# Kernel optimization log

Measured on AMD Instinct MI355X. Metric: run time of the kernel, lower is better.

The kernel has to match this reference:

```python
import jax, jax.numpy as jnp
import numpy as np

N, E, B = 50000, 800000, 2000
EMB, FEAT, L, NTASK = 300, 512, 5, 1
EPS = 1e-5


def setup_inputs() -> dict:
    key = jax.random.key(0)
    ks = jax.random.split(key, 40)
    s = 0.05
    d = {
        'x': jax.random.randint(ks[0], (N, 42), 0, 3),
        'edge_index': jax.random.randint(ks[1], (2, E), 0, N),
        'edge_attr': jax.random.randint(ks[2], (E, 10), 0, 3),
        'batch': jnp.sort(jax.random.randint(ks[3], (N,), 0, B)),
        'x_add': jax.random.normal(ks[4], (B, 200), jnp.float32),
        # atom embeddings
        'atom_e1': jax.random.normal(ks[5], (120, EMB), jnp.float32) * s,
        'atom_e2': jax.random.normal(ks[6], (3, EMB), jnp.float32) * s,
        'atom_w3': jax.random.normal(ks[7], (40, EMB), jnp.float32) * s,
        'atom_b3': jnp.zeros((EMB,), jnp.float32),
        # per-layer GINEConv params (stacked over L layers)
        'edge_e1': jax.random.normal(ks[8], (L, 6, EMB), jnp.float32) * s,
        'edge_e2': jax.random.normal(ks[9], (L, 4, EMB), jnp.float32) * s,
        'edge_w3': jax.random.normal(ks[10], (L, 8, EMB), jnp.float32) * s,
        'edge_b3': jnp.zeros((L, EMB), jnp.float32),
        'mlp_w1': jax.random.normal(ks[11], (L, EMB, 2 * EMB), jnp.float32) * s,
        'mlp_b1': jnp.zeros((L, 2 * EMB), jnp.float32),
        'mlp_w2': jax.random.normal(ks[12], (L, 2 * EMB, EMB), jnp.float32) * s,
        'mlp_b2': jnp.zeros((L, EMB), jnp.float32),
        'bn_g': jnp.ones((L, EMB), jnp.float32),
        'bn_b': jnp.zeros((L, EMB), jnp.float32),
        # feat_lin: emb_dim + 200 -> feat_dim
        'feat_w': jax.random.normal(ks[13], (EMB + 200, FEAT), jnp.float32) * s,
        'feat_b': jnp.zeros((FEAT,), jnp.float32),
        # pred head: 512->256 softplus, 256->256 softplus, 256->1
        'pw1': jax.random.normal(ks[14], (FEAT, FEAT // 2), jnp.float32) * s,
        'pb1': jnp.zeros((FEAT // 2,), jnp.float32),
        'pw2': jax.random.normal(ks[15], (FEAT // 2, FEAT // 2), jnp.float32) * s,
        'pb2': jnp.zeros((FEAT // 2,), jnp.float32),
        'pw3': jax.random.normal(ks[16], (FEAT // 2, NTASK), jnp.float32) * s,
        'pb3': jnp.zeros((NTASK,), jnp.float32),
    }
    return d


def reference(x, edge_index, edge_attr, batch, x_add,
              atom_e1, atom_e2, atom_w3, atom_b3,
              edge_e1, edge_e2, edge_w3, edge_b3,
              mlp_w1, mlp_b1, mlp_w2, mlp_b2, bn_g, bn_b,
              feat_w, feat_b, pw1, pb1, pw2, pb2, pw3, pb3):
    n = x.shape[0]
    nb = x_add.shape[0]

    # node embedding: emb(atom_type) + emb(chirality) + Linear(40 float feats)
    h = (atom_e1[x[:, 0]] + atom_e2[x[:, 1]]
         + x[:, 2:].astype(jnp.float32) @ atom_w3 + atom_b3)

    # add self loops once (same for every layer); self-loop attr: col0=4, rest 0
    loop = jnp.arange(n, dtype=edge_index.dtype)
    src = jnp.concatenate([edge_index[0], loop])
    dst = jnp.concatenate([edge_index[1], loop])
    ea0 = jnp.concatenate([edge_attr[:, 0], jnp.full((n,), 4, edge_attr.dtype)])
    ea1 = jnp.concatenate([edge_attr[:, 1], jnp.zeros((n,), edge_attr.dtype)])
    eaf = jnp.concatenate([edge_attr[:, 2:].astype(jnp.float32),
                           jnp.zeros((n, 8), jnp.float32)], axis=0)

    for l in range(L):
        e_emb = edge_e1[l][ea0] + edge_e2[l][ea1] + eaf @ edge_w3[l] + edge_b3[l]
        msg = h[src] + e_emb                              # [E+N, EMB] gather
        agg = jax.ops.segment_sum(msg, dst, num_segments=n)  # scatter-add
        h = jnp.maximum(agg @ mlp_w1[l] + mlp_b1[l], 0.0) @ mlp_w2[l] + mlp_b2[l]
        # BatchNorm1d (training-mode batch stats, biased var)
        mu = jnp.mean(h, axis=0)
        var = jnp.mean((h - mu) ** 2, axis=0)
        h = (h - mu) * jax.lax.rsqrt(var + EPS) * bn_g[l] + bn_b[l]
        if l != L - 1:
            h = jnp.maximum(h, 0.0)
    h_node = h

    # global mean pool per graph
    sums = jax.ops.segment_sum(h_node, batch, num_segments=nb)
    cnt = jax.ops.segment_sum(jnp.ones((n, 1), h_node.dtype), batch, num_segments=nb)
    pooled = sums / jnp.maximum(cnt, 1.0)

    g = jnp.concatenate([pooled, x_add], axis=1) @ feat_w + feat_b
    g = jax.nn.softplus(g @ pw1 + pb1)
    g = jax.nn.softplus(g @ pw2 + pb2)
    pred = g @ pw3 + pb3
    return h_node, pred
```

## Files before the change

### kernel.cpp

```cpp
#include <hip/hip_runtime.h>
#include <stdint.h>

#define NN 50000
#define EE 800000
#define BG 2000
#define EMB 300
#define HP 320
#define YP 640
#define MPAD 50048
#define MHEAD 2048
#define NLAYER 5

typedef __attribute__((ext_vector_type(8))) _Float16 f16x8;
typedef __attribute__((ext_vector_type(4))) float f32x4;

__device__ __forceinline__ _Float16 f2h(float f) { return (_Float16)f; }

__global__ void k_tconv_all(const float* __restrict__ mw1, const float* __restrict__ mw2,
        const float* __restrict__ fw, const float* __restrict__ pw1, const float* __restrict__ pw2,
        _Float16* __restrict__ w1t, _Float16* __restrict__ w2t, _Float16* __restrict__ fwt,
        _Float16* __restrict__ p1t, _Float16* __restrict__ p2t) {
    int job = blockIdx.x;
    const float* src; _Float16* dst; int K, Ns, Kp, Np;
    if (job < 5)       { src = mw1 + (size_t)job * EMB * 2 * EMB; dst = w1t + (size_t)job * YP * HP; K = EMB; Ns = 2 * EMB; Kp = HP; Np = YP; }
    else if (job < 10) { int l = job - 5; src = mw2 + (size_t)l * 2 * EMB * EMB; dst = w2t + (size_t)l * HP * YP; K = 2 * EMB; Ns = EMB; Kp = YP; Np = HP; }
    else if (job == 10){ src = fw;  dst = fwt; K = 500; Ns = 512; Kp = 512; Np = 512; }
    else if (job == 11){ src = pw1; dst = p1t; K = 512; Ns = 256; Kp = 512; Np = 256; }
    else               { src = pw2; dst = p2t; K = 256; Ns = 256; Kp = 256; Np = 256; }
    int total = Kp * Np;
    for (int idx = blockIdx.y * 256 + threadIdx.x; idx < total; idx += gridDim.y * 256) {
        int n = idx / Kp, k = idx - n * Kp;
        float v = (n < Ns && k < K) ? src[(size_t)k * Ns + n] : 0.f;
        dst[idx] = f2h(v);
    }
}

__global__ void k_padbias_all(const float* __restrict__ mb1, const float* __restrict__ mb2,
                              float* __restrict__ b1p, float* __restrict__ b2p) {
    int idx = blockIdx.x * 256 + threadIdx.x;
    if (idx < NLAYER * YP) {
        int l = idx / YP, c = idx - l * YP;
        b1p[idx] = (c < 2 * EMB) ? mb1[(size_t)l * 2 * EMB + c] : 0.f;
    } else if (idx < NLAYER * YP + NLAYER * HP) {
        int j = idx - NLAYER * YP; int l = j / HP, c = j - l * HP;
        b2p[j] = (c < EMB) ? mb2[(size_t)l * EMB + c] : 0.f;
    }
}

__global__ void k_prep(int* __restrict__ deg, int* __restrict__ cursor,
                       float* __restrict__ psum, float* __restrict__ psq) {
    int i = blockIdx.x * blockDim.x + threadIdx.x;
    if (i < NN) { deg[i] = 0; cursor[i] = 0; }
    if (i < NLAYER * HP) { psum[i] = 0.f; psq[i] = 0.f; }
}

__global__ __launch_bounds__(256) void k_embed(const int* __restrict__ x,
        const float* __restrict__ ae1, const float* __restrict__ ae2,
        const float* __restrict__ aw3, const float* __restrict__ ab3,
        _Float16* __restrict__ h2) {
    int node = blockIdx.x * 4 + (threadIdx.x >> 6);
    int lane = threadIdx.x & 63;
    if (node >= MPAD) return;
    _Float16* outr = h2 + (size_t)node * HP;
    if (node >= NN) {
        #pragma unroll
        for (int j = 0; j < 5; j++) outr[lane + 64 * j] = (_Float16)0.f;
        return;
    }
    const int* xr = x + (size_t)node * 42;
    int x0 = xr[0], x1 = xr[1];
    float acc[5];
    #pragma unroll
    for (int j = 0; j < 5; j++) {
        int c = lane + 64 * j;
        acc[j] = (j < 4 || c < EMB)
               ? (ab3[c] + ae1[(size_t)x0 * EMB + c] + ae2[(size_t)x1 * EMB + c]) : 0.f;
    }
    for (int k = 0; k < 40; k++) {
        float xv = (float)xr[2 + k];
        #pragma unroll
        for (int j = 0; j < 5; j++) {
            int c = lane + 64 * j;
            if (j < 4 || c < EMB) acc[j] = fmaf(xv, aw3[(size_t)k * EMB + c], acc[j]);
        }
    }
    #pragma unroll
    for (int j = 0; j < 5; j++) {
        int c = lane + 64 * j;
        outr[c] = (j < 4 || c < EMB) ? f2h(acc[j]) : (_Float16)0.f;
    }
}

__global__ void k_deg(const int* __restrict__ ei, int* __restrict__ deg) {
    int e = blockIdx.x * blockDim.x + threadIdx.x;
    if (e < EE) atomicAdd(&deg[ei[EE + e]], 1);
}

__global__ __launch_bounds__(1024) void k_scan(const int* __restrict__ deg,
                                               int* __restrict__ rowptr) {
    __shared__ int part[1024];
    int t = threadIdx.x;
    const int chunk = (NN + 1023) / 1024;
    int i0 = t * chunk;
    int i1 = min(i0 + chunk, NN);
    int s = 0;
    for (int i = i0; i < i1; i++) s += deg[i];
    part[t] = s;
    __syncthreads();
    for (int off = 1; off < 1024; off <<= 1) {
        int v = part[t];
        int u = (t >= off) ? part[t - off] : 0;
        __syncthreads();
        part[t] = v + u;
        __syncthreads();
    }
    int run = (t > 0) ? part[t - 1] : 0;
    for (int i = i0; i < i1; i++) { rowptr[i] = run; run += deg[i]; }
    if (t == 1023) rowptr[NN] = part[1023];
}

__global__ void k_fill(const int* __restrict__ ei, const int* __restrict__ ea,
                       const int* __restrict__ rowptr, int* __restrict__ cursor,
                       int* __restrict__ col, unsigned int* __restrict__ eattr) {
    int e = blockIdx.x * blockDim.x + threadIdx.x;
    if (e < EE) {
        int d = ei[EE + e];
        int pos = rowptr[d] + atomicAdd(&cursor[d], 1);
        col[pos] = ei[e];
        unsigned int p = (unsigned int)ea[e * 10 + 0] | ((unsigned int)ea[e * 10 + 1] << 2);
        #pragma unroll
        for (int j = 0; j < 8; j++) p |= (unsigned int)ea[e * 10 + 2 + j] << (4 + 2 * j);
        eattr[pos] = p;
    }
}

__global__ __launch_bounds__(256) void k_sortrows(const int* __restrict__ rowptr,
                                                  int* __restrict__ col) {
    int node = blockIdx.x * 4 + (threadIdx.x >> 6);
    int lane = threadIdx.x & 63;
    if (node >= NN) return;
    int beg = rowptr[node], end = rowptr[node + 1];
    int deg = end - beg;
    if (deg <= 1 || deg > 64) return;
    int v = (lane < deg) ? col[beg + lane] : 0x7fffffff;
    #pragma unroll
    for (int k = 2; k <= 64; k <<= 1) {
        #pragma unroll
        for (int j = k >> 1; j > 0; j >>= 1) {
            int v2 = __shfl_xor(v, j);
            bool keepMin = (((lane & j) == 0) == ((lane & k) == 0));
            v = keepMin ? min(v, v2) : max(v, v2);
        }
    }
    if (lane < deg) col[beg + lane] = v;
}

__global__ __launch_bounds__(256) void k_stats(const int* __restrict__ rowptr,
        const unsigned int* __restrict__ eattr, int* __restrict__ stat) {
    int node = blockIdx.x * 4 + (threadIdx.x >> 6);
    int lane = threadIdx.x & 63;
    if (node >= NN) return;
    int beg = rowptr[node], end = rowptr[node + 1];
    int c0 = 0, c1 = 0, c2 = 0, d1 = 0, d2 = 0;
    int s[8] = {0, 0, 0, 0, 0, 0, 0, 0};
    for (int e = beg + lane; e < end; e += 64) {
        unsigned int p = eattr[e];
        unsigned int a0 = p & 3u, a1 = (p >> 2) & 3u;
        c0 += (a0 == 0); c1 += (a0 == 1); c2 += (a0 == 2);
        d1 += (a1 == 1); d2 += (a1 == 2);
        #pragma unroll
        for (int j = 0; j < 8; j++) s[j] += (int)((p >> (4 + 2 * j)) & 3u);
    }
    #pragma unroll
    for (int off = 32; off; off >>= 1) {
        c0 += __shfl_down(c0, off); c1 += __shfl_down(c1, off); c2 += __shfl_down(c2, off);
        d1 += __shfl_down(d1, off); d2 += __shfl_down(d2, off);
        #pragma unroll
        for (int j = 0; j < 8; j++) s[j] += __shfl_down(s[j], off);
    }
    if (lane == 0) {
        int dg = end - beg;
        int* st = stat + (size_t)node * 20;
        st[0] = c0; st[1] = c1; st[2] = c2; st[3] = 0; st[4] = 1; st[5] = 0;
        st[6] = dg - d1 - d2 + 1; st[7] = d1; st[8] = d2; st[9] = 0;
        #pragma unroll
        for (int j = 0; j < 8; j++) st[10 + j] = s[j];
        st[18] = dg + 1; st[19] = 0;
    }
}

#define AGG_CHUNK 160
template<int RELU>
__global__ __launch_bounds__(320) void k_agg(const _Float16* __restrict__ h2,
        const float* __restrict__ psum, const float* __restrict__ psq,
        const float* __restrict__ bng, const float* __restrict__ bnb,
        const int* __restrict__ stat, const int* __restrict__ rowptr,
        const int* __restrict__ col,
        const float* __restrict__ ee1, const float* __restrict__ ee2,
        const float* __restrict__ ew3, const float* __restrict__ eb3,
        _Float16* __restrict__ agg, int layer) {
    int i = blockIdx.x;
    int tid = threadIdx.x;
    if (i >= NN) { agg[(size_t)i * HP + tid] = (_Float16)0.f; return; }
    __shared__ int ss[20];
    __shared__ int sc[AGG_CHUNK];
    if (tid < 20) ss[tid] = stat[(size_t)i * 20 + tid];
    int c = tid;
    bool ch = c < EMB;
    float scl = 0.f, sft = 0.f;
    if (ch) {
        if (RELU) {
            float mu = psum[(size_t)(layer - 1) * HP + c] * (1.f / NN);
            float var = psq[(size_t)(layer - 1) * HP + c] * (1.f / NN) - mu * mu;
            float g = bng[(size_t)(layer - 1) * EMB + c] * rsqrtf(var + 1e-5f);
            scl = g; sft = bnb[(size_t)(layer - 1) * EMB + c] - mu * g;
        } else { scl = 1.f; sft = 0.f; }
    }
    __syncthreads();
    float acc = 0.f;
    if (ch) {
        const float* e1 = ee1 + (size_t)layer * 6 * EMB;
        const float* e2 = ee2 + (size_t)layer * 4 * EMB;
        const float* w3 = ew3 + (size_t)layer * 8 * EMB;
        float v = eb3[(size_t)layer * EMB + c] * (float)ss[18] + e1[4 * EMB + c];
        v = fmaf((float)ss[0], e1[c], v);
        v = fmaf((float)ss[1], e1[EMB + c], v);
        v = fmaf((float)ss[2], e1[2 * EMB + c], v);
        v = fmaf((float)ss[6], e2[c], v);
        v = fmaf((float)ss[7], e2[EMB + c], v);
        v = fmaf((float)ss[8], e2[2 * EMB + c], v);
        #pragma unroll
        for (int k = 0; k < 8; k++) v = fmaf((float)ss[10 + k], w3[k * EMB + c], v);
        float t = fmaf((float)h2[(size_t)i * HP + c], scl, sft);
        if (RELU) t = fmaxf(t, 0.f);
        acc = v + t;
    }
    int beg = rowptr[i], end = rowptr[i + 1];
    for (int e0 = beg; e0 < end; e0 += AGG_CHUNK) {
        int m = min(AGG_CHUNK, end - e0);
        __syncthreads();
        if (tid < m) sc[tid] = col[e0 + tid];
        __syncthreads();
        if (ch) {
            #pragma unroll 4
            for (int e = 0; e < m; e++) {
                float t = fmaf((float)h2[(size_t)sc[e] * HP + c], scl, sft);
                if (RELU) t = fmaxf(t, 0.f);
                acc += t;
            }
        }
    }
    agg[(size_t)i * HP + tid] = ch ? f2h(acc) : (_Float16)0.f;
}

__global__ __launch_bounds__(256) void k_gemm(const _Float16* __restrict__ A, int lda,
        const _Float16* __restrict__ Wt, int ldw, const float* __restrict__ bias,
        _Float16* __restrict__ C, int ldc, int K, int act, int gridY,
        float* __restrict__ psum, float* __restrict__ psq) {
    __shared__ _Float16 As[2][128 * 32];
    __shared__ _Float16 Bs[2][64 * 32];
    int nwg = gridDim.x;
    int q = nwg >> 3, r = nwg & 7;
    int xcd = blockIdx.x & 7, idx = blockIdx.x >> 3;
    int wg = ((xcd < r) ? xcd * (q + 1) : r * (q + 1) + (xcd - r) * q) + idx;
    int bx = wg / gridY, by = wg - bx * gridY;
    size_t rowBase = (size_t)bx * 128;
    int colBase = by * 64;

    int tid = threadIdx.x, lane = tid & 63, wid = tid >> 6;
    int wr = wid >> 1, wc = wid & 1;
    int srow = tid >> 2, schunk = tid & 3;
    int gchunk = schunk ^ ((srow >> 1) & 3);
    const _Float16* Ab  = A + (rowBase + srow) * (size_t)lda + (gchunk << 3);
    const _Float16* Ab2 = Ab + (size_t)64 * lda;
    const _Float16* Bb  = Wt + ((size_t)colBase + srow) * ldw + (gchunk << 3);
    int ldsbase = wid << 9;

    int lr = lane & 15, lg = lane >> 4;
    int lswz = (lr >> 1) & 3;
    int aoff[4], boff[2];
    #pragma unroll
    for (int m = 0; m < 4; m++) { int rr = wr * 64 + m * 16 + lr; aoff[m] = rr * 32 + ((lg ^ lswz) << 3); }
    #pragma unroll
    for (int n = 0; n < 2; n++) { int rr = wc * 32 + n * 16 + lr; boff[n] = rr * 32 + ((lg ^ lswz) << 3); }

    f32x4 acc[4][2];
    #pragma unroll
    for (int m = 0; m < 4; m++)
        #pragma unroll
        for (int n = 0; n < 2; n++) acc[m][n] = (f32x4){0.f, 0.f, 0.f, 0.f};

    auto stage = [&](int buf, int kt) {
        int o = kt << 5;
        __builtin_amdgcn_global_load_lds(
            (const __attribute__((address_space(1))) void*)(Ab + o),
            (__attribute__((address_space(3))) void*)&As[buf][ldsbase], 16, 0, 0);
        __builtin_amdgcn_global_load_lds(
            (const __attribute__((address_space(1))) void*)(Ab2 + o),
            (__attribute__((address_space(3))) void*)&As[buf][64 * 32 + ldsbase], 16, 0, 0);
        __builtin_amdgcn_global_load_lds(
            (const __attribute__((address_space(1))) void*)(Bb + o),
            (__attribute__((address_space(3))) void*)&Bs[buf][ldsbase], 16, 0, 0);
    };

    int nk = K >> 5;
    stage(0, 0);
    __syncthreads();
    int cur = 0;
    for (int kt = 0; kt < nk; ++kt) {
        if (kt + 1 < nk) stage(cur ^ 1, kt + 1);
        f16x8 af[4], bfr[2];
        #pragma unroll
        for (int m = 0; m < 4; m++) af[m] = *(const f16x8*)&As[cur][aoff[m]];
        #pragma unroll
        for (int n = 0; n < 2; n++) bfr[n] = *(const f16x8*)&Bs[cur][boff[n]];
        #pragma unroll
        for (int m = 0; m < 4; m++)
            #pragma unroll
            for (int n = 0; n < 2; n++)
                acc[m][n] = __builtin_amdgcn_mfma_f32_16x16x32_f16(af[m], bfr[n], acc[m][n], 0, 0, 0);
        __syncthreads();
        cur ^= 1;
    }

    bool dostats = (psum != nullptr);
    float sstat[2] = {0.f, 0.f}, qstat[2] = {0.f, 0.f};
    #pragma unroll
    for (int m = 0; m < 4; m++) {
        #pragma unroll
        for (int n = 0; n < 2; n++) {
            int colg = colBase + wc * 32 + n * 16 + lr;
            float bv = bias[colg];
            #pragma unroll
            for (int rj = 0; rj < 4; rj++) {
                size_t rowg = rowBase + wr * 64 + m * 16 + lg * 4 + rj;
                float v = acc[m][n][rj] + bv;
                if (act == 1) v = fmaxf(v, 0.f);
                else if (act == 2) v = (v > 0.f) ? v + log1pf(expf(-v)) : log1pf(expf(v));
                C[rowg * ldc + colg] = f2h(v);
                if (dostats && rowg < NN) { sstat[n] += v; qstat[n] += v * v; }
            }
        }
    }
    if (dostats) {
        #pragma unroll
        for (int n = 0; n < 2; n++) {
            float s_ = sstat[n], q_ = qstat[n];
            s_ += __shfl_xor(s_, 16); q_ += __shfl_xor(q_, 16);
            s_ += __shfl_xor(s_, 32); q_ += __shfl_xor(q_, 32);
            if (lane < 16) {
                int colg = colBase + wc * 32 + n * 16 + lr;
                atomicAdd(&psum[colg], s_);
                atomicAdd(&psq[colg], q_);
            }
        }
    }
}

__global__ __launch_bounds__(256) void k_bn_apply(const _Float16* __restrict__ h2,
        const float* __restrict__ psum, const float* __restrict__ psq,
        const float* __restrict__ bng, const float* __restrict__ bnb,
        float* __restrict__ out) {
    int node = blockIdx.x * 4 + (threadIdx.x >> 6);
    int lane = threadIdx.x & 63;
    if (node >= NN) return;
    const float* ps = psum + (size_t)(NLAYER - 1) * HP;
    const float* pq = psq  + (size_t)(NLAYER - 1) * HP;
    const float* g_ = bng + (size_t)(NLAYER - 1) * EMB;
    const float* b_ = bnb + (size_t)(NLAYER - 1) * EMB;
    #pragma unroll
    for (int j = 0; j < 5; j++) {
        int c = lane + 64 * j;
        if (j < 4 || c < EMB) {
            float mu = ps[c] * (1.f / NN);
            float var = pq[c] * (1.f / NN) - mu * mu;
            float g = g_[c] * rsqrtf(var + 1e-5f);
            out[(size_t)node * EMB + c] =
                fmaf((float)h2[(size_t)node * HP + c], g, b_[c] - mu * g);
        }
    }
}

__global__ __launch_bounds__(512) void k_pool(const float* __restrict__ hn,
        const int* __restrict__ batch, const float* __restrict__ x_add,
        _Float16* __restrict__ hin) {
    int b = blockIdx.x, c = threadIdx.x;
    if (b >= BG) { hin[(size_t)b * 512 + c] = (_Float16)0.f; return; }
    __shared__ int sb[2];
    if (c < 2) {
        int target = b + c;
        int lo = 0, hi = NN;
        while (lo < hi) { int mid = (lo + hi) >> 1; if (batch[mid] < target) lo = mid + 1; else hi = mid; }
        sb[c] = lo;
    }
    __syncthreads();
    float v = 0.f;
    if (c < EMB) {
        int s = sb[0], e = sb[1];
        float a = 0.f;
        for (int i = s; i < e; i++) a += hn[(size_t)i * EMB + c];
        v = a / (float)max(e - s, 1);
    } else if (c < EMB + 200) {
        v = x_add[(size_t)b * 200 + (c - EMB)];
    }
    hin[(size_t)b * 512 + c] = f2h(v);
}

__global__ __launch_bounds__(64) void k_pred(const _Float16* __restrict__ g3,
        const float* __restrict__ pw3, const float* __restrict__ pb3, float* __restrict__ out) {
    int row = blockIdx.x;
    int lane = threadIdx.x;
    float s = 0.f;
    #pragma unroll
    for (int t = 0; t < 4; t++) {
        int k = lane * 4 + t;
        s += (float)g3[(size_t)row * 256 + k] * pw3[k];
    }
    #pragma unroll
    for (int off = 32; off; off >>= 1) s += __shfl_down(s, off);
    if (lane == 0) out[row] = s + pb3[0];
}

extern "C" void kernel_launch(void* const* d_in, const int* in_sizes, int n_in,
                              void* d_out, int out_size, void* d_ws, size_t ws_size,
                              hipStream_t stream) {
    const int*   x     = (const int*)d_in[0];
    const int*   ei    = (const int*)d_in[1];
    const int*   ea    = (const int*)d_in[2];
    const int*   batch = (const int*)d_in[3];
    const float* x_add = (const float*)d_in[4];
    const float* ae1   = (const float*)d_in[5];
    const float* ae2   = (const float*)d_in[6];
    const float* aw3   = (const float*)d_in[7];
    const float* ab3   = (const float*)d_in[8];
    const float* ee1   = (const float*)d_in[9];
    const float* ee2   = (const float*)d_in[10];
    const float* ew3   = (const float*)d_in[11];
    const float* eb3   = (const float*)d_in[12];
    const float* mw1   = (const float*)d_in[13];
    const float* mb1   = (const float*)d_in[14];
    const float* mw2   = (const float*)d_in[15];
    const float* mb2   = (const float*)d_in[16];
    const float* bng   = (const float*)d_in[17];
    const float* bnb   = (const float*)d_in[18];
    const float* fw    = (const float*)d_in[19];
    const float* fb    = (const float*)d_in[20];
    const float* pw1   = (const float*)d_in[21];
    const float* pb1   = (const float*)d_in[22];
    const float* pw2   = (const float*)d_in[23];
    const float* pb2   = (const float*)d_in[24];
    const float* pw3   = (const float*)d_in[25];
    const float* pb3   = (const float*)d_in[26];
    (void)in_sizes; (void)n_in; (void)out_size; (void)ws_size;
    float* out = (float*)d_out;

    char* p = (char*)d_ws;
    auto take = [&](size_t bytes) -> char* {
        char* r = p; p += (bytes + 255) & ~(size_t)255; return r;
    };
    _Float16*  h2   = (_Float16*)take((size_t)MPAD * HP * 2);
    _Float16*  agg  = (_Float16*)take((size_t)MPAD * HP * 2);
    _Float16*  y1   = (_Float16*)take((size_t)MPAD * YP * 2);
    _Float16*  w1t  = (_Float16*)take((size_t)NLAYER * YP * HP * 2);
    _Float16*  w2t  = (_Float16*)take((size_t)NLAYER * HP * YP * 2);
    _Float16*  fwt  = (_Float16*)take((size_t)512 * 512 * 2);
    _Float16*  p1t  = (_Float16*)take((size_t)256 * 512 * 2);
    _Float16*  p2t  = (_Float16*)take((size_t)256 * 256 * 2);
    float* b1p    = (float*)take((size_t)NLAYER * YP * 4);
    float* b2p    = (float*)take((size_t)NLAYER * HP * 4);
    int* deg      = (int*)take((size_t)NN * 4);
    int* cursor   = (int*)take((size_t)NN * 4);
    int* rowptr   = (int*)take((size_t)(NN + 1) * 4);
    int* col      = (int*)take((size_t)EE * 4);
    unsigned int* eattr = (unsigned int*)take((size_t)EE * 4);
    int* stat     = (int*)take((size_t)NN * 20 * 4);
    float* psum   = (float*)take((size_t)NLAYER * HP * 4);
    float* psq    = (float*)take((size_t)NLAYER * HP * 4);
    char* hb = (char*)y1;
    _Float16* hin = (_Float16*)hb;  hb += (size_t)MHEAD * 512 * 2;
    _Float16* g1  = (_Float16*)hb;  hb += (size_t)MHEAD * 512 * 2;
    _Float16* g2  = (_Float16*)hb;  hb += (size_t)MHEAD * 256 * 2;
    _Float16* g3  = (_Float16*)hb;

    k_prep<<<(NN + 255) / 256, 256, 0, stream>>>(deg, cursor, psum, psq);
    k_tconv_all<<<dim3(13, 1024), 256, 0, stream>>>(mw1, mw2, fw, pw1, pw2, w1t, w2t, fwt, p1t, p2t);
    k_padbias_all<<<19, 256, 0, stream>>>(mb1, mb2, b1p, b2p);
    k_embed<<<(MPAD + 3) / 4, 256, 0, stream>>>(x, ae1, ae2, aw3, ab3, h2);
    k_deg<<<(EE + 255) / 256, 256, 0, stream>>>(ei, deg);
    k_scan<<<1, 1024, 0, stream>>>(deg, rowptr);
    k_fill<<<(EE + 255) / 256, 256, 0, stream>>>(ei, ea, rowptr, cursor, col, eattr);
    k_sortrows<<<(NN + 3) / 4, 256, 0, stream>>>(rowptr, col);
    k_stats<<<(NN + 3) / 4, 256, 0, stream>>>(rowptr, eattr, stat);

    const int MT = MPAD / 128;
    for (int l = 0; l < NLAYER; l++) {
        if (l == 0)
            k_agg<0><<<MPAD, 320, 0, stream>>>(h2, psum, psq, bng, bnb,
                stat, rowptr, col, ee1, ee2, ew3, eb3, agg, l);
        else
            k_agg<1><<<MPAD, 320, 0, stream>>>(h2, psum, psq, bng, bnb,
                stat, rowptr, col, ee1, ee2, ew3, eb3, agg, l);
        k_gemm<<<MT * (YP / 64), 256, 0, stream>>>(
            agg, HP, w1t + (size_t)l * YP * HP, HP, b1p + (size_t)l * YP,
            y1, YP, HP, 1, YP / 64, nullptr, nullptr);
        k_gemm<<<MT * (HP / 64), 256, 0, stream>>>(
            y1, YP, w2t + (size_t)l * HP * YP, YP, b2p + (size_t)l * HP,
            h2, HP, YP, 0, HP / 64, psum + (size_t)l * HP, psq + (size_t)l * HP);
    }
    k_bn_apply<<<(NN + 3) / 4, 256, 0, stream>>>(h2, psum, psq, bng, bnb, out);

    k_pool<<<MHEAD, 512, 0, stream>>>(out, batch, x_add, hin);
    k_gemm<<<(MHEAD / 128) * (512 / 64), 256, 0, stream>>>(hin, 512, fwt, 512, fb, g1, 512, 512, 0, 512 / 64, nullptr, nullptr);
    k_gemm<<<(MHEAD / 128) * (256 / 64), 256, 0, stream>>>(g1, 512, p1t, 512, pb1, g2, 256, 512, 2, 256 / 64, nullptr, nullptr);
    k_gemm<<<(MHEAD / 128) * (256 / 64), 256, 0, stream>>>(g2, 256, p2t, 256, pb2, g3, 256, 256, 2, 256 / 64, nullptr, nullptr);
    k_pred<<<BG, 64, 0, stream>>>(g3, pw3, pb3, out + (size_t)NN * EMB);
}
```

Before: 1.815 ms.

## Widen GEMM tiles to 128x128, unroll aggregation gathers, drop row sorting

The GEMM tile grows from 128x64 to 128x128, so each wave holds a 4x4 grid of MFMA accumulators. The padded N dimension is masked with an Nvalid bound, and the W2 transpose is padded to 384 rows so it covers three 128-wide column tiles. The aggregation kernel now loads neighbour indices straight from global memory and issues eight gathers at a time instead of staging them through shared memory with barriers. The per-row column sort kernel is removed. This changes the summation order, and dropping the sort may hurt gather locality, while the larger tiles raise register pressure and give the second GEMM fewer blocks.

```diff
diff --git a/kernel.cpp b/kernel.cpp
--- a/kernel.cpp
+++ b/kernel.cpp
@@ -7,6 +7,7 @@
 #define EMB 300
 #define HP 320
 #define YP 640
+#define W2ROWS 384
 #define MPAD 50048
 #define MHEAD 2048
 #define NLAYER 5
@@ -23,7 +24,7 @@
     int job = blockIdx.x;
     const float* src; _Float16* dst; int K, Ns, Kp, Np;
     if (job < 5)       { src = mw1 + (size_t)job * EMB * 2 * EMB; dst = w1t + (size_t)job * YP * HP; K = EMB; Ns = 2 * EMB; Kp = HP; Np = YP; }
-    else if (job < 10) { int l = job - 5; src = mw2 + (size_t)l * 2 * EMB * EMB; dst = w2t + (size_t)l * HP * YP; K = 2 * EMB; Ns = EMB; Kp = YP; Np = HP; }
+    else if (job < 10) { int l = job - 5; src = mw2 + (size_t)l * 2 * EMB * EMB; dst = w2t + (size_t)l * W2ROWS * YP; K = 2 * EMB; Ns = EMB; Kp = YP; Np = W2ROWS; }
     else if (job == 10){ src = fw;  dst = fwt; K = 500; Ns = 512; Kp = 512; Np = 512; }
     else if (job == 11){ src = pw1; dst = p1t; K = 512; Ns = 256; Kp = 512; Np = 256; }
     else               { src = pw2; dst = p2t; K = 256; Ns = 256; Kp = 256; Np = 256; }
@@ -134,27 +135,6 @@
     }
 }
 
-__global__ __launch_bounds__(256) void k_sortrows(const int* __restrict__ rowptr,
-                                                  int* __restrict__ col) {
-    int node = blockIdx.x * 4 + (threadIdx.x >> 6);
-    int lane = threadIdx.x & 63;
-    if (node >= NN) return;
-    int beg = rowptr[node], end = rowptr[node + 1];
-    int deg = end - beg;
-    if (deg <= 1 || deg > 64) return;
-    int v = (lane < deg) ? col[beg + lane] : 0x7fffffff;
-    #pragma unroll
-    for (int k = 2; k <= 64; k <<= 1) {
-        #pragma unroll
-        for (int j = k >> 1; j > 0; j >>= 1) {
-            int v2 = __shfl_xor(v, j);
-            bool keepMin = (((lane & j) == 0) == ((lane & k) == 0));
-            v = keepMin ? min(v, v2) : max(v, v2);
-        }
-    }
-    if (lane < deg) col[beg + lane] = v;
-}
-
 __global__ __launch_bounds__(256) void k_stats(const int* __restrict__ rowptr,
         const unsigned int* __restrict__ eattr, int* __restrict__ stat) {
     int node = blockIdx.x * 4 + (threadIdx.x >> 6);
@@ -189,7 +169,6 @@
     }
 }
 
-#define AGG_CHUNK 160
 template<int RELU>
 __global__ __launch_bounds__(320) void k_agg(const _Float16* __restrict__ h2,
         const float* __restrict__ psum, const float* __restrict__ psq,
@@ -203,7 +182,6 @@
     int tid = threadIdx.x;
     if (i >= NN) { agg[(size_t)i * HP + tid] = (_Float16)0.f; return; }
     __shared__ int ss[20];
-    __shared__ int sc[AGG_CHUNK];
     if (tid < 20) ss[tid] = stat[(size_t)i * 20 + tid];
     int c = tid;
     bool ch = c < EMB;
@@ -231,41 +209,52 @@
         v = fmaf((float)ss[8], e2[2 * EMB + c], v);
         #pragma unroll
         for (int k = 0; k < 8; k++) v = fmaf((float)ss[10 + k], w3[k * EMB + c], v);
+        acc = v;
+    }
+    {
         float t = fmaf((float)h2[(size_t)i * HP + c], scl, sft);
         if (RELU) t = fmaxf(t, 0.f);
-        acc = v + t;
+        acc += t;
     }
     int beg = rowptr[i], end = rowptr[i + 1];
-    for (int e0 = beg; e0 < end; e0 += AGG_CHUNK) {
-        int m = min(AGG_CHUNK, end - e0);
-        __syncthreads();
-        if (tid < m) sc[tid] = col[e0 + tid];
-        __syncthreads();
-        if (ch) {
-            #pragma unroll 4
-            for (int e = 0; e < m; e++) {
-                float t = fmaf((float)h2[(size_t)sc[e] * HP + c], scl, sft);
-                if (RELU) t = fmaxf(t, 0.f);
-                acc += t;
-            }
+    int e = beg;
+    for (; e + 8 <= end; e += 8) {
+        int cb[8];
+        #pragma unroll
+        for (int t = 0; t < 8; t++) cb[t] = col[e + t];
+        float vb[8];
+        #pragma unroll
+        for (int t = 0; t < 8; t++) vb[t] = (float)h2[(size_t)cb[t] * HP + c];
+        float tb[8];
+        #pragma unroll
+        for (int t = 0; t < 8; t++) {
+            float tt = fmaf(vb[t], scl, sft);
+            if (RELU) tt = fmaxf(tt, 0.f);
+            tb[t] = tt;
         }
-    }
-    agg[(size_t)i * HP + tid] = ch ? f2h(acc) : (_Float16)0.f;
+        acc += ((tb[0] + tb[1]) + (tb[2] + tb[3])) + ((tb[4] + tb[5]) + (tb[6] + tb[7]));
+    }
+    for (; e < end; ++e) {
+        float tt = fmaf((float)h2[(size_t)col[e] * HP + c], scl, sft);
+        if (RELU) tt = fmaxf(tt, 0.f);
+        acc += tt;
+    }
+    agg[(size_t)i * HP + tid] = f2h(acc);
 }
 
 __global__ __launch_bounds__(256) void k_gemm(const _Float16* __restrict__ A, int lda,
         const _Float16* __restrict__ Wt, int ldw, const float* __restrict__ bias,
-        _Float16* __restrict__ C, int ldc, int K, int act, int gridY,
+        _Float16* __restrict__ C, int ldc, int Nvalid, int K, int act, int gridY,
         float* __restrict__ psum, float* __restrict__ psq) {
     __shared__ _Float16 As[2][128 * 32];
-    __shared__ _Float16 Bs[2][64 * 32];
+    __shared__ _Float16 Bs[2][128 * 32];
     int nwg = gridDim.x;
     int q = nwg >> 3, r = nwg & 7;
     int xcd = blockIdx.x & 7, idx = blockIdx.x >> 3;
     int wg = ((xcd < r) ? xcd * (q + 1) : r * (q + 1) + (xcd - r) * q) + idx;
     int bx = wg / gridY, by = wg - bx * gridY;
     size_t rowBase = (size_t)bx * 128;
-    int colBase = by * 64;
+    int colBase = by * 128;
 
     int tid = threadIdx.x, lane = tid & 63, wid = tid >> 6;
     int wr = wid >> 1, wc = wid & 1;
@@ -274,21 +263,22 @@
     const _Float16* Ab  = A + (rowBase + srow) * (size_t)lda + (gchunk << 3);
     const _Float16* Ab2 = Ab + (size_t)64 * lda;
     const _Float16* Bb  = Wt + ((size_t)colBase + srow) * ldw + (gchunk << 3);
+    const _Float16* Bb2 = Bb + (size_t)64 * ldw;
     int ldsbase = wid << 9;
 
     int lr = lane & 15, lg = lane >> 4;
     int lswz = (lr >> 1) & 3;
-    int aoff[4], boff[2];
+    int aoff[4], boff[4];
     #pragma unroll
     for (int m = 0; m < 4; m++) { int rr = wr * 64 + m * 16 + lr; aoff[m] = rr * 32 + ((lg ^ lswz) << 3); }
     #pragma unroll
-    for (int n = 0; n < 2; n++) { int rr = wc * 32 + n * 16 + lr; boff[n] = rr * 32 + ((lg ^ lswz) << 3); }
-
-    f32x4 acc[4][2];
+    for (int n = 0; n < 4; n++) { int rr = wc * 64 + n * 16 + lr; boff[n] = rr * 32 + ((lg ^ lswz) << 3); }
+
+    f32x4 acc[4][4];
     #pragma unroll
     for (int m = 0; m < 4; m++)
         #pragma unroll
-        for (int n = 0; n < 2; n++) acc[m][n] = (f32x4){0.f, 0.f, 0.f, 0.f};
+        for (int n = 0; n < 4; n++) acc[m][n] = (f32x4){0.f, 0.f, 0.f, 0.f};
 
     auto stage = [&](int buf, int kt) {
         int o = kt << 5;
@@ -301,6 +291,9 @@
         __builtin_amdgcn_global_load_lds(
             (const __attribute__((address_space(1))) void*)(Bb + o),
             (__attribute__((address_space(3))) void*)&Bs[buf][ldsbase], 16, 0, 0);
+        __builtin_amdgcn_global_load_lds(
+            (const __attribute__((address_space(1))) void*)(Bb2 + o),
+            (__attribute__((address_space(3))) void*)&Bs[buf][64 * 32 + ldsbase], 16, 0, 0);
     };
 
     int nk = K >> 5;
@@ -309,49 +302,45 @@
     int cur = 0;
     for (int kt = 0; kt < nk; ++kt) {
         if (kt + 1 < nk) stage(cur ^ 1, kt + 1);
-        f16x8 af[4], bfr[2];
+        f16x8 af[4], bf[4];
         #pragma unroll
         for (int m = 0; m < 4; m++) af[m] = *(const f16x8*)&As[cur][aoff[m]];
         #pragma unroll
-        for (int n = 0; n < 2; n++) bfr[n] = *(const f16x8*)&Bs[cur][boff[n]];
+        for (int n = 0; n < 4; n++) bf[n] = *(const f16x8*)&Bs[cur][boff[n]];
         #pragma unroll
         for (int m = 0; m < 4; m++)
             #pragma unroll
-            for (int n = 0; n < 2; n++)
-                acc[m][n] = __builtin_amdgcn_mfma_f32_16x16x32_f16(af[m], bfr[n], acc[m][n], 0, 0, 0);
+            for (int n = 0; n < 4; n++)
+                acc[m][n] = __builtin_amdgcn_mfma_f32_16x16x32_f16(af[m], bf[n], acc[m][n], 0, 0, 0);
         __syncthreads();
         cur ^= 1;
     }
 
     bool dostats = (psum != nullptr);
-    float sstat[2] = {0.f, 0.f}, qstat[2] = {0.f, 0.f};
-    #pragma unroll
-    for (int m = 0; m < 4; m++) {
-        #pragma unroll
-        for (int n = 0; n < 2; n++) {
-            int colg = colBase + wc * 32 + n * 16 + lr;
-            float bv = bias[colg];
+    #pragma unroll
+    for (int n = 0; n < 4; n++) {
+        int colg = colBase + wc * 64 + n * 16 + lr;
+        bool cok = colg < Nvalid;
+        float bv = cok ? bias[colg] : 0.f;
+        float sstat = 0.f, qstat = 0.f;
+        #pragma unroll
+        for (int m = 0; m < 4; m++) {
             #pragma unroll
             for (int rj = 0; rj < 4; rj++) {
                 size_t rowg = rowBase + wr * 64 + m * 16 + lg * 4 + rj;
                 float v = acc[m][n][rj] + bv;
                 if (act == 1) v = fmaxf(v, 0.f);
                 else if (act == 2) v = (v > 0.f) ? v + log1pf(expf(-v)) : log1pf(expf(v));
-                C[rowg * ldc + colg] = f2h(v);
-                if (dostats && rowg < NN) { sstat[n] += v; qstat[n] += v * v; }
+                if (cok) C[rowg * ldc + colg] = f2h(v);
+                if (dostats && rowg < NN) { sstat += v; qstat += v * v; }
             }
         }
-    }
-    if (dostats) {
-        #pragma unroll
-        for (int n = 0; n < 2; n++) {
-            float s_ = sstat[n], q_ = qstat[n];
-            s_ += __shfl_xor(s_, 16); q_ += __shfl_xor(q_, 16);
-            s_ += __shfl_xor(s_, 32); q_ += __shfl_xor(q_, 32);
-            if (lane < 16) {
-                int colg = colBase + wc * 32 + n * 16 + lr;
-                atomicAdd(&psum[colg], s_);
-                atomicAdd(&psq[colg], q_);
+        if (dostats) {
+            sstat += __shfl_xor(sstat, 16); qstat += __shfl_xor(qstat, 16);
+            sstat += __shfl_xor(sstat, 32); qstat += __shfl_xor(qstat, 32);
+            if (lane < 16 && cok) {
+                atomicAdd(&psum[colg], sstat);
+                atomicAdd(&psq[colg], qstat);
             }
         }
     }
@@ -462,7 +451,7 @@
     _Float16*  agg  = (_Float16*)take((size_t)MPAD * HP * 2);
     _Float16*  y1   = (_Float16*)take((size_t)MPAD * YP * 2);
     _Float16*  w1t  = (_Float16*)take((size_t)NLAYER * YP * HP * 2);
-    _Float16*  w2t  = (_Float16*)take((size_t)NLAYER * HP * YP * 2);
+    _Float16*  w2t  = (_Float16*)take((size_t)NLAYER * W2ROWS * YP * 2);
     _Float16*  fwt  = (_Float16*)take((size_t)512 * 512 * 2);
     _Float16*  p1t  = (_Float16*)take((size_t)256 * 512 * 2);
     _Float16*  p2t  = (_Float16*)take((size_t)256 * 256 * 2);
@@ -489,7 +478,6 @@
     k_deg<<<(EE + 255) / 256, 256, 0, stream>>>(ei, deg);
     k_scan<<<1, 1024, 0, stream>>>(deg, rowptr);
     k_fill<<<(EE + 255) / 256, 256, 0, stream>>>(ei, ea, rowptr, cursor, col, eattr);
-    k_sortrows<<<(NN + 3) / 4, 256, 0, stream>>>(rowptr, col);
     k_stats<<<(NN + 3) / 4, 256, 0, stream>>>(rowptr, eattr, stat);
 
     const int MT = MPAD / 128;
@@ -500,18 +488,18 @@
         else
             k_agg<1><<<MPAD, 320, 0, stream>>>(h2, psum, psq, bng, bnb,
                 stat, rowptr, col, ee1, ee2, ew3, eb3, agg, l);
-        k_gemm<<<MT * (YP / 64), 256, 0, stream>>>(
+        k_gemm<<<MT * 5, 256, 0, stream>>>(
             agg, HP, w1t + (size_t)l * YP * HP, HP, b1p + (size_t)l * YP,
-            y1, YP, HP, 1, YP / 64, nullptr, nullptr);
-        k_gemm<<<MT * (HP / 64), 256, 0, stream>>>(
-            y1, YP, w2t + (size_t)l * HP * YP, YP, b2p + (size_t)l * HP,
-            h2, HP, YP, 0, HP / 64, psum + (size_t)l * HP, psq + (size_t)l * HP);
+            y1, YP, YP, HP, 1, 5, nullptr, nullptr);
+        k_gemm<<<MT * 3, 256, 0, stream>>>(
+            y1, YP, w2t + (size_t)l * W2ROWS * YP, YP, b2p + (size_t)l * HP,
+            h2, HP, HP, YP, 0, 3, psum + (size_t)l * HP, psq + (size_t)l * HP);
     }
     k_bn_apply<<<(NN + 3) / 4, 256, 0, stream>>>(h2, psum, psq, bng, bnb, out);
 
     k_pool<<<MHEAD, 512, 0, stream>>>(out, batch, x_add, hin);
-    k_gemm<<<(MHEAD / 128) * (512 / 64), 256, 0, stream>>>(hin, 512, fwt, 512, fb, g1, 512, 512, 0, 512 / 64, nullptr, nullptr);
-    k_gemm<<<(MHEAD / 128) * (256 / 64), 256, 0, stream>>>(g1, 512, p1t, 512, pb1, g2, 256, 512, 2, 256 / 64, nullptr, nullptr);
-    k_gemm<<<(MHEAD / 128) * (256 / 64), 256, 0, stream>>>(g2, 256, p2t, 256, pb2, g3, 256, 256, 2, 256 / 64, nullptr, nullptr);
+    k_gemm<<<(MHEAD / 128) * 4, 256, 0, stream>>>(hin, 512, fwt, 512, fb, g1, 512, 512, 512, 0, 4, nullptr, nullptr);
+    k_gemm<<<(MHEAD / 128) * 2, 256, 0, stream>>>(g1, 512, p1t, 512, pb1, g2, 256, 256, 512, 2, 2, nullptr, nullptr);
+    k_gemm<<<(MHEAD / 128) * 2, 256, 0, stream>>>(g2, 256, p2t, 256, pb2, g3, 256, 256, 256, 2, 2, nullptr, nullptr);
     k_pred<<<BG, 64, 0, stream>>>(g3, pw3, pb3, out + (size_t)NN * EMB);
 }
```

Result: slower. 2.126 ms (+17.1%).
